# Optimization experiments

Hardware: AMD Instinct MI355X
Metric: run time of the kernel (lower is better)

The kernel has to match this reference:

```python
import jax, jax.numpy as jnp
import numpy as np

NEG = 1e9


def setup_inputs() -> dict:
    key = jax.random.key(0)
    ks = jax.random.split(key, 12)
    B, T1, T2, D1, D2, O, KF, G = 32, 512, 512, 256, 256, 256, 8, 64
    s = jnp.float32(0.05)  # keras 'random_normal' initializer stddev
    x0 = jax.random.normal(ks[0], (B, T1, D1), jnp.float32)
    x1 = jax.random.normal(ks[1], (B, T2, D2), jnp.float32)
    # realistic padding masks: first len tokens valid
    len1 = jax.random.randint(ks[2], (B,), T1 // 2, T1 + 1)
    len2 = jax.random.randint(ks[3], (B,), T2 // 2, T2 + 1)
    q_mask = jnp.arange(T1)[None, :] < len1[:, None]
    v_mask = jnp.arange(T2)[None, :] < len2[:, None]
    return {
        "x0": x0, "x1": x1, "q_mask": q_mask, "v_mask": v_mask,
        "W_R": jax.random.normal(ks[4], (1, O, D1), jnp.float32) * s,
        "W_Q": jax.random.normal(ks[5], (1, O, D2), jnp.float32) * s,
        "br": jnp.zeros((O, 1), jnp.float32),
        "bq": jnp.zeros((O, 1), jnp.float32),
        "U": jax.random.normal(ks[6], (1, O, T2, KF), jnp.float32) * s,
        "V": jax.random.normal(ks[7], (1, O, T1, KF), jnp.float32) * s,
        "W2_R": jax.random.normal(ks[8], (1, G, O), jnp.float32) * s,
        "W2_Q": jax.random.normal(ks[9], (1, G, O), jnp.float32) * s,
        "w_mv": jax.random.normal(ks[10], (G, 1), jnp.float32) * s,
        "w_mq": jax.random.normal(ks[11], (G, 1), jnp.float32) * s,
    }


def reference(x0, x1, q_mask, v_mask, W_R, W_Q, br, bq, U, V, W2_R, W2_Q, w_mv, w_mq):
    B, T1, D1 = x0.shape
    _, T2, D2 = x1.shape
    O = W_R.shape[1]
    KF = U.shape[-1]
    dt = x0.dtype
    # NB: original uses tf.reshape (NOT transpose) for all axis swaps; replicate exactly.
    in1 = x0.reshape(B, D1, T1)
    in2 = x1.reshape(B, D2, T2)
    R_l = jnp.einsum('od,bdt->bot', W_R[0], in1)          # (B,O,T1)
    Q_l = jnp.einsum('od,bds->bos', W_Q[0], in2)          # (B,O,T2)
    pad_q = (~q_mask).astype(dt)                          # (B,T1)
    pad_v = (~v_mask).astype(dt)                          # (B,T2)
    R_l = R_l - NEG * pad_q[:, None, :]
    Q_l = Q_l - NEG * pad_v[:, None, :]
    R_l = jax.nn.relu(R_l + br[None])                     # br (O,1) broadcasts over T1
    Q_l = jax.nn.relu(Q_l + bq[None])
    # factorized bilinear interaction, vectorized over rank k
    Uk = jnp.moveaxis(U[0], -1, 0).reshape(KF, T2, O)     # per-k reshape (O,T2)->(T2,O)
    Vk = jnp.moveaxis(V[0], -1, 0).reshape(KF, T1, O)     # per-k reshape (O,T1)->(T1,O)
    dot1 = jnp.einsum('kto,bos->kbts', Uk, R_l)           # (k,B,T2,T1)
    dot1 = dot1.reshape(KF, B, T1, T2)                    # per-slice reshape (T2,T1)->(T1,T2)
    dot2 = jnp.einsum('kso,bot->kbst', Vk, Q_l)           # (k,B,T1,T2)
    F = jnp.sum(dot1 * dot2, axis=0)                      # (B,T1,T2)
    F_tr = F.reshape(B, T2, T1)
    WR = jnp.einsum('go,bot->bgt', W2_R[0], R_l)          # (B,G,T1)
    WQ = jnp.einsum('go,bos->bgs', W2_Q[0], Q_l)          # (B,G,T2)
    M_v = jax.nn.relu(WR + jnp.einsum('bgs,bst->bgt', WQ, F_tr))   # (B,G,T1)
    M_q = jax.nn.relu(WQ + jnp.einsum('bgt,bts->bgs', WR, F))      # (B,G,T2)
    d1 = jnp.einsum('g,bgt->bt', w_mv[:, 0], M_v) - NEG * pad_q    # (B,T1)
    d2 = jnp.einsum('g,bgs->bs', w_mq[:, 0], M_q) - NEG * pad_v    # (B,T2)
    gamma_v = jax.nn.softmax(d1, axis=-1)
    gamma_q = jax.nn.softmax(d2, axis=-1)
    R_l2 = R_l.reshape(B, T1, O)
    Q_l2 = Q_l.reshape(B, T2, O)
    trace_emb = jnp.einsum('bt,bto->bo', gamma_v, R_l2)
    log_emb = jnp.einsum('bs,bso->bo', gamma_q, Q_l2)
    return trace_emb * log_emb                            # (B,O)
```

## Files before the change

kernel.cpp:

```cpp
#include <hip/hip_runtime.h>
#include <hip/hip_bf16.h>

typedef __hip_bfloat16 bf16;
typedef short bf16x8 __attribute__((ext_vector_type(8)));
typedef float f32x4 __attribute__((ext_vector_type(4)));
typedef unsigned int u32x4 __attribute__((ext_vector_type(4)));
typedef unsigned short us4 __attribute__((ext_vector_type(4)));

#define NEGV 1e9f

static constexpr int Bn = 32, Tn = 512, Dn = 256, On = 256, KFn = 8, Gn = 64;

__device__ __forceinline__ float bfs2f(unsigned short s) {
    unsigned u = ((unsigned)s) << 16; float f; __builtin_memcpy(&f, &u, 4); return f;
}
__device__ __forceinline__ unsigned short f2bfs(float f) {
    unsigned u; __builtin_memcpy(&u, &f, 4);
    u = u + 0x7FFFu + ((u >> 16) & 1u);
    return (unsigned short)(u >> 16);
}
__device__ __forceinline__ float loadf(const void* p, int i, int fl) {
    return fl ? bfs2f(((const unsigned short*)p)[i]) : ((const float*)p)[i];
}
__device__ __forceinline__ int detect_flag(const void* x0) {
    const unsigned short* u = (const unsigned short*)x0;
    int bad = 0;
    for (int i = 0; i < 32; i++) {
        unsigned short v = u[2 * i];
        int e = (v >> 7) & 0xFF;
        if (!(v == 0 || (e >= 90 && e <= 150))) bad++;
    }
    return (bad == 0) ? 1 : 0;
}
__device__ __forceinline__ void gload16(const unsigned short* g, unsigned short* l) {
    __builtin_amdgcn_global_load_lds(
        (const __attribute__((address_space(1))) unsigned int*)(unsigned long long)g,
        (__attribute__((address_space(3))) unsigned int*)(unsigned int)(unsigned long long)l,
        16, 0, 0);
}

__global__ void k_prep(const void* __restrict__ x0,
                       const void* __restrict__ qm, const void* __restrict__ vm,
                       const void* __restrict__ W_R, const void* __restrict__ W_Q,
                       const void* __restrict__ br, const void* __restrict__ bq,
                       const void* __restrict__ W2R, const void* __restrict__ W2Q,
                       const void* __restrict__ wmv, const void* __restrict__ wmq,
                       int* __restrict__ flag, float* __restrict__ padq, float* __restrict__ padv,
                       float* __restrict__ brf, float* __restrict__ bqf,
                       float* __restrict__ wmvf, float* __restrict__ wmqf,
                       float* __restrict__ W2Rf, float* __restrict__ W2Qf,
                       unsigned short* __restrict__ Whr, unsigned short* __restrict__ Wlr,
                       unsigned short* __restrict__ Whq, unsigned short* __restrict__ Wlq) {
    const int fl = detect_flag(x0);
    const int bid = blockIdx.x, tid = threadIdx.x;
    if (bid == 0) {
        if (tid == 0) *flag = fl;
        brf[tid] = loadf(br, tid, fl);
        bqf[tid] = loadf(bq, tid, fl);
        if (tid < 64) { wmvf[tid] = loadf(wmv, tid, fl); wmqf[tid] = loadf(wmq, tid, fl); }
    } else if (bid <= 128) {
        int i = (bid - 1) * 256 + tid;
        const unsigned char* qb = (const unsigned char*)qm;
        bool is32 = (qb[1] == 0);
        int j = i & 16383;
        const void* m = (i < 16384) ? qm : vm;
        float pv;
        if (is32) pv = ((const int*)m)[j] ? 0.f : 1.f;
        else      pv = ((const unsigned char*)m)[j] ? 0.f : 1.f;
        if (i < 16384) padq[j] = pv; else padv[j] = pv;
    } else if (bid <= 640) {
        int i = (bid - 129) * 256 + tid;
        const void* src = (i < 65536) ? W_R : W_Q;
        unsigned short* oh = (i < 65536) ? Whr : Whq;
        unsigned short* ol = (i < 65536) ? Wlr : Wlq;
        int j = i & 65535;
        float wv = loadf(src, j, fl);
        unsigned short h = f2bfs(wv);
        oh[j] = h;
        ol[j] = f2bfs(wv - bfs2f(h));
    } else {
        int i = (bid - 641) * 256 + tid;
        int j = i & 16383;
        if (i < 16384) W2Rf[j] = loadf(W2R, j, fl);
        else           W2Qf[j] = loadf(W2Q, j, fl);
    }
}

__global__ void k_perm(const void* __restrict__ U, const void* __restrict__ V,
                       unsigned short* __restrict__ Ud, unsigned short* __restrict__ Vd,
                       const int* __restrict__ flagp) {
    int i = blockIdx.x * 256 + threadIdx.x;
    const void* src = blockIdx.y ? V : U;
    unsigned short* dst = blockIdx.y ? Vd : Ud;
    int o = i & 255;
    int m = i >> 8;
    int a = m >> 3, k = m & 7;
    int f = a * 256 + o;
    int s = ((f >> 9) << 12) + ((f & 511) << 3) + k;
    if (*flagp) dst[i] = ((const unsigned short*)src)[s];
    else        dst[i] = f2bfs(((const float*)src)[s]);
}

__global__ __launch_bounds__(256) void k_xt(
    const void* __restrict__ x0, const void* __restrict__ x1,
    unsigned short* __restrict__ X0h, unsigned short* __restrict__ X0l,
    unsigned short* __restrict__ X1h, unsigned short* __restrict__ X1l,
    const int* __restrict__ flagp) {
    __shared__ float tl[64][65];
    const int inp = blockIdx.z >> 5, b = blockIdx.z & 31;
    const void* src = inp ? x1 : x0;
    unsigned short* oh = inp ? X1h : X0h;
    unsigned short* ol = inp ? X1l : X0l;
    const int t0 = blockIdx.x * 64, d0 = blockIdx.y * 64;
    const int tid = threadIdx.x;
    const int fl = *flagp;
#pragma unroll
    for (int p = 0; p < 16; ++p) {
        int idx = p * 256 + tid;
        int r = idx >> 6, c = idx & 63;
        size_t gi = ((size_t)b * 256 + d0 + r) * 512 + t0 + c;
        tl[r][c] = fl ? bfs2f(((const unsigned short*)src)[gi]) : ((const float*)src)[gi];
    }
    __syncthreads();
#pragma unroll
    for (int p = 0; p < 16; ++p) {
        int idx = p * 256 + tid;
        int r = idx >> 6, c = idx & 63;
        float v = tl[c][r];
        unsigned short h = f2bfs(v);
        size_t go = ((size_t)b * 512 + t0 + r) * 256 + d0 + c;
        oh[go] = h;
        ol[go] = f2bfs(v - bfs2f(h));
    }
}

__global__ __launch_bounds__(256) void k_rq(
    const unsigned short* __restrict__ X0h, const unsigned short* __restrict__ X0l,
    const unsigned short* __restrict__ X1h, const unsigned short* __restrict__ X1l,
    const unsigned short* __restrict__ Whr, const unsigned short* __restrict__ Wlr,
    const unsigned short* __restrict__ Whq, const unsigned short* __restrict__ Wlq,
    const float* __restrict__ padq, const float* __restrict__ padv,
    const float* __restrict__ brf, const float* __restrict__ bqf,
    unsigned short* __restrict__ Rth, unsigned short* __restrict__ Rtl,
    unsigned short* __restrict__ Qth, unsigned short* __restrict__ Qtl) {
    __shared__ __align__(16) unsigned short lds[4][4096];
    const int side = blockIdx.z >> 5, b = blockIdx.z & 31;
    const unsigned short* Ah = side ? X1h : X0h;
    const unsigned short* Al = side ? X1l : X0l;
    const unsigned short* Bh = side ? Whq : Whr;
    const unsigned short* Bl = side ? Wlq : Wlr;
    const float* pad = side ? padv : padq;
    const float* bias = side ? bqf : brf;
    unsigned short* Oh = side ? Qth : Rth;
    unsigned short* Ol = side ? Qtl : Rtl;
    const int t0 = blockIdx.y * 128, o0 = blockIdx.x * 128;
    const int tid = threadIdx.x, w = tid >> 6, lane = tid & 63;
    const int wm = w >> 1, wn = w & 1, lr = lane & 15, lk = lane >> 4;
    f32x4 acc[4][4];
#pragma unroll
    for (int i = 0; i < 4; i++)
#pragma unroll
        for (int j = 0; j < 4; j++)
#pragma unroll
            for (int q = 0; q < 4; q++) acc[i][j][q] = 0.f;

    for (int dc = 0; dc < 8; ++dc) {
        const int d0 = dc * 32;
        __syncthreads();
#pragma unroll
        for (int part = 0; part < 2; ++part) {
            const int s = w + part * 4;
            const size_t oA = ((size_t)(b * 512 + t0 + s * 16 + lr)) * 256 + d0 + lk * 8;
            const size_t oB = ((size_t)(o0 + s * 16 + lr)) * 256 + d0 + lk * 8;
            unsigned short* lb = &lds[0][s * 512];
            gload16(Ah + oA, lb);
            gload16(Al + oA, lb + 4096);
            gload16(Bh + oB, lb + 8192);
            gload16(Bl + oB, lb + 12288);
        }
        __syncthreads();
        bf16x8 ah[4], bh[4], bl[4], al[4];
#pragma unroll
        for (int f = 0; f < 4; ++f) {
            ah[f] = *(const bf16x8*)&lds[0][(wm * 4 + f) * 512 + lane * 8];
            bh[f] = *(const bf16x8*)&lds[2][(wn * 4 + f) * 512 + lane * 8];
        }
#pragma unroll
        for (int fa = 0; fa < 4; ++fa)
#pragma unroll
            for (int fc = 0; fc < 4; ++fc)
                acc[fa][fc] = __builtin_amdgcn_mfma_f32_16x16x32_bf16(ah[fa], bh[fc], acc[fa][fc], 0, 0, 0);
#pragma unroll
        for (int f = 0; f < 4; ++f)
            bl[f] = *(const bf16x8*)&lds[3][(wn * 4 + f) * 512 + lane * 8];
#pragma unroll
        for (int fa = 0; fa < 4; ++fa)
#pragma unroll
            for (int fc = 0; fc < 4; ++fc)
                acc[fa][fc] = __builtin_amdgcn_mfma_f32_16x16x32_bf16(ah[fa], bl[fc], acc[fa][fc], 0, 0, 0);
#pragma unroll
        for (int f = 0; f < 4; ++f)
            al[f] = *(const bf16x8*)&lds[1][(wm * 4 + f) * 512 + lane * 8];
#pragma unroll
        for (int fa = 0; fa < 4; ++fa)
#pragma unroll
            for (int fc = 0; fc < 4; ++fc)
                acc[fa][fc] = __builtin_amdgcn_mfma_f32_16x16x32_bf16(al[fa], bh[fc], acc[fa][fc], 0, 0, 0);
    }
    float bi[4];
#pragma unroll
    for (int fn = 0; fn < 4; ++fn) bi[fn] = bias[o0 + wn * 64 + fn * 16 + lr];
#pragma unroll
    for (int fm = 0; fm < 4; ++fm) {
        int tbase = t0 + wm * 64 + fm * 16 + lk * 4;
#pragma unroll
        for (int q = 0; q < 4; ++q) {
            int t = tbase + q;
            float pv = NEGV * pad[b * 512 + t];
#pragma unroll
            for (int fn = 0; fn < 4; ++fn) {
                int o = o0 + wn * 64 + fn * 16 + lr;
                float v = acc[fm][fn][q] - pv + bi[fn];
                v = v > 0.f ? v : 0.f;
                unsigned short h = f2bfs(v);
                size_t off = ((size_t)(b * 512 + t)) * 256 + o;
                Oh[off] = h;
                Ol[off] = f2bfs(v - bfs2f(h));
            }
        }
    }
}

__global__ __launch_bounds__(256, 2) void k_F(
    const unsigned short* __restrict__ Upp, const unsigned short* __restrict__ Vpp,
    const unsigned short* __restrict__ Rh, const unsigned short* __restrict__ Rl,
    const unsigned short* __restrict__ Qh, const unsigned short* __restrict__ Ql,
    float* __restrict__ Fh, int half) {
    __shared__ __align__(16) unsigned short lds[32][512];
    const int b = blockIdx.z;
    const int by = blockIdx.y;
    const int c0 = blockIdx.x * 64;
    const int m0 = half * 2048 + by * 128;
    const int tid = threadIdx.x;
    const int w = tid >> 6, lane = tid & 63;
    const int wm = w >> 1, wn = w & 1;
    const int lr = lane & 15, lk = lane >> 4;
    const size_t bTO = (size_t)b * Tn * On;

    const size_t aoff0 = (size_t)(m0 + (2 * w) * 16 + lr) * 256 + lk * 8;
    const size_t aoff1 = aoff0 + 16 * 256;
    const size_t boff = bTO + (size_t)(c0 + w * 16 + lr) * 256 + lk * 8;

    f32x4 d1[4][2], d2[4][2];
#pragma unroll
    for (int i = 0; i < 4; i++)
#pragma unroll
        for (int j = 0; j < 2; j++)
#pragma unroll
            for (int q = 0; q < 4; q++) { d1[i][j][q] = 0.f; d2[i][j][q] = 0.f; }

    for (int oc = 0; oc < 8; ++oc) {
        const int o0 = oc * 32;
        __syncthreads();
        gload16(Upp + aoff0 + o0, &lds[2 * w][0]);
        gload16(Upp + aoff1 + o0, &lds[2 * w + 1][0]);
        gload16(Vpp + aoff0 + o0, &lds[8 + 2 * w][0]);
        gload16(Vpp + aoff1 + o0, &lds[8 + 2 * w + 1][0]);
        gload16(Rh + boff + o0, &lds[16 + w][0]);
        gload16(Rl + boff + o0, &lds[20 + w][0]);
        gload16(Qh + boff + o0, &lds[24 + w][0]);
        gload16(Ql + boff + o0, &lds[28 + w][0]);
        __syncthreads();
        {
            bf16x8 ua[4], xh[2], xl[2];
#pragma unroll
            for (int f = 0; f < 4; ++f)
                ua[f] = *(const bf16x8*)&lds[wm * 4 + f][lane * 8];
#pragma unroll
            for (int f = 0; f < 2; ++f) {
                xh[f] = *(const bf16x8*)&lds[16 + wn * 2 + f][lane * 8];
                xl[f] = *(const bf16x8*)&lds[20 + wn * 2 + f][lane * 8];
            }
#pragma unroll
            for (int fa = 0; fa < 4; ++fa)
#pragma unroll
                for (int fc = 0; fc < 2; ++fc) {
                    d1[fa][fc] = __builtin_amdgcn_mfma_f32_16x16x32_bf16(ua[fa], xh[fc], d1[fa][fc], 0, 0, 0);
                    d1[fa][fc] = __builtin_amdgcn_mfma_f32_16x16x32_bf16(ua[fa], xl[fc], d1[fa][fc], 0, 0, 0);
                }
        }
        {
            bf16x8 va[4], xh[2], xl[2];
#pragma unroll
            for (int f = 0; f < 4; ++f)
                va[f] = *(const bf16x8*)&lds[8 + wm * 4 + f][lane * 8];
#pragma unroll
            for (int f = 0; f < 2; ++f) {
                xh[f] = *(const bf16x8*)&lds[24 + wn * 2 + f][lane * 8];
                xl[f] = *(const bf16x8*)&lds[28 + wn * 2 + f][lane * 8];
            }
#pragma unroll
            for (int fa = 0; fa < 4; ++fa)
#pragma unroll
                for (int fc = 0; fc < 2; ++fc) {
                    d2[fa][fc] = __builtin_amdgcn_mfma_f32_16x16x32_bf16(va[fa], xh[fc], d2[fa][fc], 0, 0, 0);
                    d2[fa][fc] = __builtin_amdgcn_mfma_f32_16x16x32_bf16(va[fa], xl[fc], d2[fa][fc], 0, 0, 0);
                }
        }
    }
#pragma unroll
    for (int fa = 0; fa < 4; ++fa)
#pragma unroll
        for (int fc = 0; fc < 2; ++fc) {
            float s = d1[fa][fc][0] * d2[fa][fc][0] + d1[fa][fc][1] * d2[fa][fc][1]
                    + d1[fa][fc][2] * d2[fa][fc][2] + d1[fa][fc][3] * d2[fa][fc][3];
            s += __shfl_xor(s, 16);
            if ((lane & 16) == 0) {
                int a_loc = by * 16 + wm * 8 + fa * 2 + (lk >> 1);
                int c = c0 + wn * 32 + fc * 16 + lr;
                Fh[((size_t)b * 256 + a_loc) * Tn + c] = s;
            }
        }
}

__global__ __launch_bounds__(256) void k_w2(
    const float* __restrict__ W2Rf, const float* __restrict__ W2Qf,
    const unsigned short* __restrict__ Rth, const unsigned short* __restrict__ Rtl,
    const unsigned short* __restrict__ Qth, const unsigned short* __restrict__ Qtl,
    float* __restrict__ WRw, float* __restrict__ WQw) {
    __shared__ float Wl[32][68];
    __shared__ float Sl[32][68];
    const int side = blockIdx.z;
    const float* W2 = side ? W2Qf : W2Rf;
    const unsigned short* Sh = side ? Qth : Rth;
    const unsigned short* Sl2 = side ? Qtl : Rtl;
    float* C = side ? WQw : WRw;
    int b = blockIdx.y, t0 = blockIdx.x * 64;
    int tid = threadIdx.x, tx = tid & 15, ty = tid >> 4;
    float acc[4][4] = {};
    for (int d0 = 0; d0 < On; d0 += 32) {
#pragma unroll
        for (int p = 0; p < 8; p++) {
            int idx = p * 256 + tid; int c = idx & 31, r = idx >> 5;
            Wl[c][r] = W2[r * On + d0 + c];
        }
#pragma unroll
        for (int p = 0; p < 8; p++) {
            int idx = p * 256 + tid; int tt = idx >> 5, c = idx & 31;
            size_t off = ((size_t)b * Tn + t0 + tt) * On + d0 + c;
            Sl[c][tt] = bfs2f(Sh[off]) + bfs2f(Sl2[off]);
        }
        __syncthreads();
#pragma unroll
        for (int kk = 0; kk < 32; kk++) {
            float4 a = *(const float4*)&Wl[kk][ty * 4];
            float4 x = *(const float4*)&Sl[kk][tx * 4];
            float av[4] = {a.x, a.y, a.z, a.w};
            float xv[4] = {x.x, x.y, x.z, x.w};
#pragma unroll
            for (int i = 0; i < 4; i++)
#pragma unroll
                for (int j = 0; j < 4; j++) acc[i][j] += av[i] * xv[j];
        }
        __syncthreads();
    }
#pragma unroll
    for (int i = 0; i < 4; i++) {
        float4 st = make_float4(acc[i][0], acc[i][1], acc[i][2], acc[i][3]);
        *(float4*)&C[((size_t)b * Gn + ty * 4 + i) * Tn + t0 + tx * 4] = st;
    }
}

__global__ __launch_bounds__(256) void k_md_acc(
    const float* __restrict__ WQw, const float* __restrict__ WRw,
    const float* __restrict__ F, float* __restrict__ Mv, float* __restrict__ Mq,
    int half, int init) {
    __shared__ float Wl1[32][68], Wl2[32][68], Fl[32][68];
    int b = blockIdx.y, x0 = blockIdx.x * 64;
    int tid = threadIdx.x, tx = tid & 15, ty = tid >> 4;
    float a1[4][4] = {}, a2[4][4] = {};
    const float* Fb = F + (size_t)b * 256 * Tn;
    for (int r0 = 0; r0 < 256; r0 += 32) {
#pragma unroll
        for (int p = 0; p < 8; p++) {
            int idx = p * 256 + tid; int c = idx & 31, g = idx >> 5;
            int rg = half * 256 + r0 + c;
            Wl1[c][g] = WQw[((size_t)b * Gn + g) * Tn + rg];
            Wl2[c][g] = WRw[((size_t)b * Gn + g) * Tn + rg];
        }
#pragma unroll
        for (int p = 0; p < 8; p++) {
            int idx = p * 256 + tid; int xx = idx & 63, c = idx >> 6;
            Fl[c][xx] = Fb[(size_t)(r0 + c) * Tn + x0 + xx];
        }
        __syncthreads();
#pragma unroll
        for (int kk = 0; kk < 32; kk++) {
            float4 w1 = *(const float4*)&Wl1[kk][ty * 4];
            float4 w2 = *(const float4*)&Wl2[kk][ty * 4];
            float4 xv = *(const float4*)&Fl[kk][tx * 4];
            float W1[4] = {w1.x, w1.y, w1.z, w1.w};
            float W2a[4] = {w2.x, w2.y, w2.z, w2.w};
            float Xv[4] = {xv.x, xv.y, xv.z, xv.w};
#pragma unroll
            for (int i = 0; i < 4; i++)
#pragma unroll
                for (int j = 0; j < 4; j++) {
                    a1[i][j] += W1[i] * Xv[j];
                    a2[i][j] += W2a[i] * Xv[j];
                }
        }
        __syncthreads();
    }
#pragma unroll
    for (int i = 0; i < 4; i++) {
        size_t off = ((size_t)b * Gn + ty * 4 + i) * Tn + x0 + tx * 4;
        if (init) {
            *(float4*)&Mv[off] = make_float4(a1[i][0], a1[i][1], a1[i][2], a1[i][3]);
            *(float4*)&Mq[off] = make_float4(a2[i][0], a2[i][1], a2[i][2], a2[i][3]);
        } else {
            float4 m1 = *(float4*)&Mv[off];
            float4 m2 = *(float4*)&Mq[off];
            m1.x += a1[i][0]; m1.y += a1[i][1]; m1.z += a1[i][2]; m1.w += a1[i][3];
            m2.x += a2[i][0]; m2.y += a2[i][1]; m2.z += a2[i][2]; m2.w += a2[i][3];
            *(float4*)&Mv[off] = m1;
            *(float4*)&Mq[off] = m2;
        }
    }
}

__global__ __launch_bounds__(256) void k_tail(
    const float* __restrict__ WRw, const float* __restrict__ WQw,
    const float* __restrict__ Mv, const float* __restrict__ Mq,
    const float* __restrict__ wmvf, const float* __restrict__ wmqf,
    const float* __restrict__ padq, const float* __restrict__ padv,
    const unsigned short* __restrict__ Rh, const unsigned short* __restrict__ Rl,
    const unsigned short* __restrict__ Qh, const unsigned short* __restrict__ Ql,
    void* __restrict__ out, const int* __restrict__ flagp) {
    __shared__ float g1[512], g2[512], w1[64], w2[64];
    __shared__ float sm1[4], sm2[4], ss1[4], ss2[4];
    const int b = blockIdx.x, tid = threadIdx.x;
    if (tid < 64) { w1[tid] = wmvf[tid]; w2[tid] = wmqf[tid]; }
    __syncthreads();
    for (int x = tid; x < 512; x += 256) {
        float s1 = 0.f, s2 = 0.f;
        for (int g = 0; g < 64; ++g) {
            size_t off = ((size_t)b * 64 + g) * 512 + x;
            float m1 = WRw[off] + Mv[off]; m1 = m1 > 0.f ? m1 : 0.f;
            float m2 = WQw[off] + Mq[off]; m2 = m2 > 0.f ? m2 : 0.f;
            s1 += w1[g] * m1;
            s2 += w2[g] * m2;
        }
        g1[x] = s1 - NEGV * padq[b * 512 + x];
        g2[x] = s2 - NEGV * padv[b * 512 + x];
    }
    __syncthreads();
    float a0 = g1[tid], a1v = g1[tid + 256], b0 = g2[tid], b1v = g2[tid + 256];
    float m1 = fmaxf(a0, a1v), m2 = fmaxf(b0, b1v);
#pragma unroll
    for (int off = 32; off; off >>= 1) {
        m1 = fmaxf(m1, __shfl_xor(m1, off));
        m2 = fmaxf(m2, __shfl_xor(m2, off));
    }
    int wid = tid >> 6;
    if ((tid & 63) == 0) { sm1[wid] = m1; sm2[wid] = m2; }
    __syncthreads();
    m1 = fmaxf(fmaxf(sm1[0], sm1[1]), fmaxf(sm1[2], sm1[3]));
    m2 = fmaxf(fmaxf(sm2[0], sm2[1]), fmaxf(sm2[2], sm2[3]));
    float e10 = expf(a0 - m1), e11 = expf(a1v - m1);
    float e20 = expf(b0 - m2), e21 = expf(b1v - m2);
    float s1 = e10 + e11, s2 = e20 + e21;
#pragma unroll
    for (int off = 32; off; off >>= 1) {
        s1 += __shfl_xor(s1, off);
        s2 += __shfl_xor(s2, off);
    }
    if ((tid & 63) == 0) { ss1[wid] = s1; ss2[wid] = s2; }
    __syncthreads();
    s1 = ss1[0] + ss1[1] + ss1[2] + ss1[3];
    s2 = ss2[0] + ss2[1] + ss2[2] + ss2[3];
    float i1 = 1.f / s1, i2 = 1.f / s2;
    g1[tid] = e10 * i1; g1[tid + 256] = e11 * i1;
    g2[tid] = e20 * i2; g2[tid + 256] = e21 * i2;
    __syncthreads();
    const int o = tid;
    const size_t r0 = ((size_t)b * Tn + o) * On;
    const size_t r1 = ((size_t)b * Tn + o + 256) * On;
    float acc1 = 0.f, acc2 = 0.f;
    for (int u8 = 0; u8 < 32; ++u8) {
        u32x4 rh0 = *(const u32x4*)&Rh[r0 + u8 * 8];
        u32x4 rl0 = *(const u32x4*)&Rl[r0 + u8 * 8];
        u32x4 rh1 = *(const u32x4*)&Rh[r1 + u8 * 8];
        u32x4 rl1 = *(const u32x4*)&Rl[r1 + u8 * 8];
        u32x4 qh0 = *(const u32x4*)&Qh[r0 + u8 * 8];
        u32x4 ql0 = *(const u32x4*)&Ql[r0 + u8 * 8];
        u32x4 qh1 = *(const u32x4*)&Qh[r1 + u8 * 8];
        u32x4 ql1 = *(const u32x4*)&Ql[r1 + u8 * 8];
#pragma unroll
        for (int e = 0; e < 4; ++e) {
            int ulo = u8 * 8 + 2 * e, uhi = ulo + 1;
            float r0lo = bfs2f((unsigned short)(rh0[e] & 0xFFFF)) + bfs2f((unsigned short)(rl0[e] & 0xFFFF));
            float r0hi = bfs2f((unsigned short)(rh0[e] >> 16))   + bfs2f((unsigned short)(rl0[e] >> 16));
            float r1lo = bfs2f((unsigned short)(rh1[e] & 0xFFFF)) + bfs2f((unsigned short)(rl1[e] & 0xFFFF));
            float r1hi = bfs2f((unsigned short)(rh1[e] >> 16))   + bfs2f((unsigned short)(rl1[e] >> 16));
            acc1 += g1[2 * ulo] * r0lo + g1[2 * uhi] * r0hi;
            acc1 += g1[2 * ulo + 1] * r1lo + g1[2 * uhi + 1] * r1hi;
            float q0lo = bfs2f((unsigned short)(qh0[e] & 0xFFFF)) + bfs2f((unsigned short)(ql0[e] & 0xFFFF));
            float q0hi = bfs2f((unsigned short)(qh0[e] >> 16))   + bfs2f((unsigned short)(ql0[e] >> 16));
            float q1lo = bfs2f((unsigned short)(qh1[e] & 0xFFFF)) + bfs2f((unsigned short)(ql1[e] & 0xFFFF));
            float q1hi = bfs2f((unsigned short)(qh1[e] >> 16))   + bfs2f((unsigned short)(ql1[e] >> 16));
            acc2 += g2[2 * ulo] * q0lo + g2[2 * uhi] * q0hi;
            acc2 += g2[2 * ulo + 1] * q1lo + g2[2 * uhi + 1] * q1hi;
        }
    }
    float p = acc1 * acc2;
    if (*flagp) ((bf16*)out)[b * On + o] = __float2bfloat16(p);
    else        ((float*)out)[b * On + o] = p;
}

extern "C" void kernel_launch(void* const* d_in, const int* in_sizes, int n_in,
                              void* d_out, int out_size, void* d_ws, size_t ws_size,
                              hipStream_t stream) {
    (void)in_sizes; (void)n_in; (void)out_size; (void)ws_size;
    const void* x0  = d_in[0];
    const void* x1  = d_in[1];
    const void* qm  = d_in[2];
    const void* vm  = d_in[3];
    const void* W_R = d_in[4];
    const void* W_Q = d_in[5];
    const void* br  = d_in[6];
    const void* bq  = d_in[7];
    const void* U   = d_in[8];
    const void* V   = d_in[9];
    const void* W2R = d_in[10];
    const void* W2Q = d_in[11];
    const void* wmv = d_in[12];
    const void* wmq = d_in[13];

    float* ws = (float*)d_ws;
    int*   flag = (int*)ws;
    float* padq = ws + 16;
    float* padv = padq + 16384;
    float* brf  = padv + 16384;
    float* bqf  = brf + 256;
    float* wmvf = bqf + 256;
    float* wmqf = wmvf + 64;
    float* W2Rf = wmqf + 64;
    float* W2Qf = W2Rf + 16384;
    unsigned short* Whr = (unsigned short*)(W2Qf + 16384);
    unsigned short* Wlr = Whr + 65536;
    unsigned short* Whq = Wlr + 65536;
    unsigned short* Wlq = Whq + 65536;
    unsigned short* Ubf = Wlq + 65536;
    unsigned short* Vbf = Ubf + 1048576;
    unsigned short* Rth = Vbf + 1048576;
    unsigned short* Rtl = Rth + 4194304;
    unsigned short* Qth = Rtl + 4194304;
    unsigned short* Qtl = Qth + 4194304;
    float* Mv   = (float*)(Qtl + 4194304);
    float* Mq   = Mv + 1048576;
    float* WRw  = Mq + 1048576;
    float* WQw  = WRw + 1048576;
    float* Fhalf = WQw + 1048576;
    unsigned short* Xt0h = (unsigned short*)Fhalf;
    unsigned short* Xt0l = Xt0h + 4194304;
    unsigned short* Xt1h = (unsigned short*)Mv;
    unsigned short* Xt1l = Xt1h + 4194304;

    k_prep<<<769, 256, 0, stream>>>(x0, qm, vm, W_R, W_Q, br, bq, W2R, W2Q, wmv, wmq,
                                    flag, padq, padv, brf, bqf, wmvf, wmqf,
                                    W2Rf, W2Qf, Whr, Wlr, Whq, Wlq);
    k_perm<<<dim3(4096, 2), 256, 0, stream>>>(U, V, Ubf, Vbf, flag);
    k_xt<<<dim3(8, 4, 64), 256, 0, stream>>>(x0, x1, Xt0h, Xt0l, Xt1h, Xt1l, flag);
    k_rq<<<dim3(2, 4, 64), 256, 0, stream>>>(Xt0h, Xt0l, Xt1h, Xt1l,
                                             Whr, Wlr, Whq, Wlq,
                                             padq, padv, brf, bqf,
                                             Rth, Rtl, Qth, Qtl);
    k_w2<<<dim3(8, 32, 2), 256, 0, stream>>>(W2Rf, W2Qf, Rth, Rtl, Qth, Qtl, WRw, WQw);
    for (int half = 0; half < 2; half++) {
        k_F<<<dim3(8, 16, 32), 256, 0, stream>>>(Ubf, Vbf, Rth, Rtl, Qth, Qtl, Fhalf, half);
        k_md_acc<<<dim3(8, 32), 256, 0, stream>>>(WQw, WRw, Fhalf, Mv, Mq, half, half == 0);
    }
    k_tail<<<32, 256, 0, stream>>>(WRw, WQw, Mv, Mq, wmvf, wmqf, padq, padv,
                                   Rth, Rtl, Qth, Qtl, d_out, flag);
}
```

Before: 514.4 us.

## Move W2 projection to split-bf16 MFMA, vectorize prep kernels, widen k_F tiles

Replaces the scalar fp32 k_w2 GEMM with an MFMA version that stores W2 as bf16 hi/lo pairs and accumulates three cross products. It also vectorizes the loads and stores in k_perm and k_xt, using 8-wide chunks. k_F moves to 512-thread blocks with a 128-column tile, so the U/V tiles are loaded once per block and shared across more columns. The aim is to cut scalar FMA and memory-transaction overhead in several kernels. The costs are larger LDS use and register pressure in k_F, and a slight precision change in WR/WQ because the lo*lo term is dropped.

```diff
diff --git a/kernel.cpp b/kernel.cpp
--- a/kernel.cpp
+++ b/kernel.cpp
@@ -5,7 +5,7 @@
 typedef short bf16x8 __attribute__((ext_vector_type(8)));
 typedef float f32x4 __attribute__((ext_vector_type(4)));
 typedef unsigned int u32x4 __attribute__((ext_vector_type(4)));
-typedef unsigned short us4 __attribute__((ext_vector_type(4)));
+typedef unsigned short us8 __attribute__((ext_vector_type(8)));
 
 #define NEGV 1e9f
 
@@ -48,7 +48,8 @@
                        int* __restrict__ flag, float* __restrict__ padq, float* __restrict__ padv,
                        float* __restrict__ brf, float* __restrict__ bqf,
                        float* __restrict__ wmvf, float* __restrict__ wmqf,
-                       float* __restrict__ W2Rf, float* __restrict__ W2Qf,
+                       unsigned short* __restrict__ W2Rh, unsigned short* __restrict__ W2Rl,
+                       unsigned short* __restrict__ W2Qh, unsigned short* __restrict__ W2Ql,
                        unsigned short* __restrict__ Whr, unsigned short* __restrict__ Wlr,
                        unsigned short* __restrict__ Whq, unsigned short* __restrict__ Wlq) {
     const int fl = detect_flag(x0);
@@ -81,24 +82,34 @@
     } else {
         int i = (bid - 641) * 256 + tid;
         int j = i & 16383;
-        if (i < 16384) W2Rf[j] = loadf(W2R, j, fl);
-        else           W2Qf[j] = loadf(W2Q, j, fl);
+        float wv = loadf(i < 16384 ? W2R : W2Q, j, fl);
+        unsigned short h = f2bfs(wv);
+        unsigned short l = f2bfs(wv - bfs2f(h));
+        if (i < 16384) { W2Rh[j] = h; W2Rl[j] = l; }
+        else           { W2Qh[j] = h; W2Ql[j] = l; }
     }
 }
 
 __global__ void k_perm(const void* __restrict__ U, const void* __restrict__ V,
                        unsigned short* __restrict__ Ud, unsigned short* __restrict__ Vd,
                        const int* __restrict__ flagp) {
-    int i = blockIdx.x * 256 + threadIdx.x;
+    int j = blockIdx.x * 256 + threadIdx.x;
     const void* src = blockIdx.y ? V : U;
     unsigned short* dst = blockIdx.y ? Vd : Ud;
-    int o = i & 255;
-    int m = i >> 8;
-    int a = m >> 3, k = m & 7;
+    int a = j >> 8, o = j & 255;
     int f = a * 256 + o;
-    int s = ((f >> 9) << 12) + ((f & 511) << 3) + k;
-    if (*flagp) dst[i] = ((const unsigned short*)src)[s];
-    else        dst[i] = f2bfs(((const float*)src)[s]);
+    int s0 = ((f >> 9) << 12) + ((f & 511) << 3);
+    unsigned short kv[8];
+    if (*flagp) {
+        us8 v = *(const us8*)&((const unsigned short*)src)[s0];
+#pragma unroll
+        for (int k = 0; k < 8; ++k) kv[k] = v[k];
+    } else {
+#pragma unroll
+        for (int k = 0; k < 8; ++k) kv[k] = f2bfs(((const float*)src)[s0 + k]);
+    }
+#pragma unroll
+    for (int k = 0; k < 8; ++k) dst[(a * 8 + k) * 256 + o] = kv[k];
 }
 
 __global__ __launch_bounds__(256) void k_xt(
@@ -115,22 +126,37 @@
     const int tid = threadIdx.x;
     const int fl = *flagp;
 #pragma unroll
-    for (int p = 0; p < 16; ++p) {
+    for (int p = 0; p < 2; ++p) {
         int idx = p * 256 + tid;
-        int r = idx >> 6, c = idx & 63;
-        size_t gi = ((size_t)b * 256 + d0 + r) * 512 + t0 + c;
-        tl[r][c] = fl ? bfs2f(((const unsigned short*)src)[gi]) : ((const float*)src)[gi];
+        int r = idx >> 3, c8 = (idx & 7) * 8;
+        size_t gi = ((size_t)b * 256 + d0 + r) * 512 + t0 + c8;
+        if (fl) {
+            us8 v = *(const us8*)&((const unsigned short*)src)[gi];
+#pragma unroll
+            for (int jj = 0; jj < 8; ++jj) tl[r][c8 + jj] = bfs2f(v[jj]);
+        } else {
+            float4 v0 = *(const float4*)&((const float*)src)[gi];
+            float4 v1 = *(const float4*)&((const float*)src)[gi + 4];
+            tl[r][c8 + 0] = v0.x; tl[r][c8 + 1] = v0.y; tl[r][c8 + 2] = v0.z; tl[r][c8 + 3] = v0.w;
+            tl[r][c8 + 4] = v1.x; tl[r][c8 + 5] = v1.y; tl[r][c8 + 6] = v1.z; tl[r][c8 + 7] = v1.w;
+        }
     }
     __syncthreads();
 #pragma unroll
-    for (int p = 0; p < 16; ++p) {
+    for (int p = 0; p < 2; ++p) {
         int idx = p * 256 + tid;
-        int r = idx >> 6, c = idx & 63;
-        float v = tl[c][r];
-        unsigned short h = f2bfs(v);
-        size_t go = ((size_t)b * 512 + t0 + r) * 256 + d0 + c;
-        oh[go] = h;
-        ol[go] = f2bfs(v - bfs2f(h));
+        int r = idx >> 3, c8 = (idx & 7) * 8;
+        us8 hv, lv;
+#pragma unroll
+        for (int jj = 0; jj < 8; ++jj) {
+            float v = tl[c8 + jj][r];
+            unsigned short h = f2bfs(v);
+            hv[jj] = h;
+            lv[jj] = f2bfs(v - bfs2f(h));
+        }
+        size_t go = ((size_t)b * 512 + t0 + r) * 256 + d0 + c8;
+        *(us8*)&oh[go] = hv;
+        *(us8*)&ol[go] = lv;
     }
 }
 
@@ -231,24 +257,23 @@
     }
 }
 
-__global__ __launch_bounds__(256, 2) void k_F(
+__global__ __launch_bounds__(512, 2) void k_F(
     const unsigned short* __restrict__ Upp, const unsigned short* __restrict__ Vpp,
     const unsigned short* __restrict__ Rh, const unsigned short* __restrict__ Rl,
     const unsigned short* __restrict__ Qh, const unsigned short* __restrict__ Ql,
     float* __restrict__ Fh, int half) {
-    __shared__ __align__(16) unsigned short lds[32][512];
+    __shared__ __align__(16) unsigned short lds[48][512];
     const int b = blockIdx.z;
     const int by = blockIdx.y;
-    const int c0 = blockIdx.x * 64;
+    const int c0 = blockIdx.x * 128;
     const int m0 = half * 2048 + by * 128;
     const int tid = threadIdx.x;
     const int w = tid >> 6, lane = tid & 63;
-    const int wm = w >> 1, wn = w & 1;
+    const int wm = w >> 2, wn = w & 3;
     const int lr = lane & 15, lk = lane >> 4;
     const size_t bTO = (size_t)b * Tn * On;
 
-    const size_t aoff0 = (size_t)(m0 + (2 * w) * 16 + lr) * 256 + lk * 8;
-    const size_t aoff1 = aoff0 + 16 * 256;
+    const size_t aoff = (size_t)(m0 + w * 16 + lr) * 256 + lk * 8;
     const size_t boff = bTO + (size_t)(c0 + w * 16 + lr) * 256 + lk * 8;
 
     f32x4 d1[4][2], d2[4][2];
@@ -262,14 +287,12 @@
     for (int oc = 0; oc < 8; ++oc) {
         const int o0 = oc * 32;
         __syncthreads();
-        gload16(Upp + aoff0 + o0, &lds[2 * w][0]);
-        gload16(Upp + aoff1 + o0, &lds[2 * w + 1][0]);
-        gload16(Vpp + aoff0 + o0, &lds[8 + 2 * w][0]);
-        gload16(Vpp + aoff1 + o0, &lds[8 + 2 * w + 1][0]);
+        gload16(Upp + aoff + o0, &lds[w][0]);
+        gload16(Vpp + aoff + o0, &lds[8 + w][0]);
         gload16(Rh + boff + o0, &lds[16 + w][0]);
-        gload16(Rl + boff + o0, &lds[20 + w][0]);
-        gload16(Qh + boff + o0, &lds[24 + w][0]);
-        gload16(Ql + boff + o0, &lds[28 + w][0]);
+        gload16(Rl + boff + o0, &lds[24 + w][0]);
+        gload16(Qh + boff + o0, &lds[32 + w][0]);
+        gload16(Ql + boff + o0, &lds[40 + w][0]);
         __syncthreads();
         {
             bf16x8 ua[4], xh[2], xl[2];
@@ -279,7 +302,7 @@
 #pragma unroll
             for (int f = 0; f < 2; ++f) {
                 xh[f] = *(const bf16x8*)&lds[16 + wn * 2 + f][lane * 8];
-                xl[f] = *(const bf16x8*)&lds[20 + wn * 2 + f][lane * 8];
+                xl[f] = *(const bf16x8*)&lds[24 + wn * 2 + f][lane * 8];
             }
 #pragma unroll
             for (int fa = 0; fa < 4; ++fa)
@@ -296,8 +319,8 @@
                 va[f] = *(const bf16x8*)&lds[8 + wm * 4 + f][lane * 8];
 #pragma unroll
             for (int f = 0; f < 2; ++f) {
-                xh[f] = *(const bf16x8*)&lds[24 + wn * 2 + f][lane * 8];
-                xl[f] = *(const bf16x8*)&lds[28 + wn * 2 + f][lane * 8];
+                xh[f] = *(const bf16x8*)&lds[32 + wn * 2 + f][lane * 8];
+                xl[f] = *(const bf16x8*)&lds[40 + wn * 2 + f][lane * 8];
             }
 #pragma unroll
             for (int fa = 0; fa < 4; ++fa)
@@ -324,51 +347,72 @@
 }
 
 __global__ __launch_bounds__(256) void k_w2(
-    const float* __restrict__ W2Rf, const float* __restrict__ W2Qf,
+    const unsigned short* __restrict__ W2Rh, const unsigned short* __restrict__ W2Rl,
+    const unsigned short* __restrict__ W2Qh, const unsigned short* __restrict__ W2Ql,
     const unsigned short* __restrict__ Rth, const unsigned short* __restrict__ Rtl,
     const unsigned short* __restrict__ Qth, const unsigned short* __restrict__ Qtl,
     float* __restrict__ WRw, float* __restrict__ WQw) {
-    __shared__ float Wl[32][68];
-    __shared__ float Sl[32][68];
-    const int side = blockIdx.z;
-    const float* W2 = side ? W2Qf : W2Rf;
-    const unsigned short* Sh = side ? Qth : Rth;
-    const unsigned short* Sl2 = side ? Qtl : Rtl;
+    __shared__ __align__(16) unsigned short lds[24][512];
+    const int side = blockIdx.z, b = blockIdx.y, t0 = blockIdx.x * 128;
+    const unsigned short* Ah = side ? W2Qh : W2Rh;
+    const unsigned short* Al = side ? W2Ql : W2Rl;
+    const unsigned short* Bh = side ? Qth : Rth;
+    const unsigned short* Bl = side ? Qtl : Rtl;
     float* C = side ? WQw : WRw;
-    int b = blockIdx.y, t0 = blockIdx.x * 64;
-    int tid = threadIdx.x, tx = tid & 15, ty = tid >> 4;
-    float acc[4][4] = {};
-    for (int d0 = 0; d0 < On; d0 += 32) {
-#pragma unroll
-        for (int p = 0; p < 8; p++) {
-            int idx = p * 256 + tid; int c = idx & 31, r = idx >> 5;
-            Wl[c][r] = W2[r * On + d0 + c];
-        }
-#pragma unroll
-        for (int p = 0; p < 8; p++) {
-            int idx = p * 256 + tid; int tt = idx >> 5, c = idx & 31;
-            size_t off = ((size_t)b * Tn + t0 + tt) * On + d0 + c;
-            Sl[c][tt] = bfs2f(Sh[off]) + bfs2f(Sl2[off]);
-        }
-        __syncthreads();
-#pragma unroll
-        for (int kk = 0; kk < 32; kk++) {
-            float4 a = *(const float4*)&Wl[kk][ty * 4];
-            float4 x = *(const float4*)&Sl[kk][tx * 4];
-            float av[4] = {a.x, a.y, a.z, a.w};
-            float xv[4] = {x.x, x.y, x.z, x.w};
-#pragma unroll
-            for (int i = 0; i < 4; i++)
-#pragma unroll
-                for (int j = 0; j < 4; j++) acc[i][j] += av[i] * xv[j];
-        }
-        __syncthreads();
-    }
-#pragma unroll
-    for (int i = 0; i < 4; i++) {
-        float4 st = make_float4(acc[i][0], acc[i][1], acc[i][2], acc[i][3]);
-        *(float4*)&C[((size_t)b * Gn + ty * 4 + i) * Tn + t0 + tx * 4] = st;
-    }
+    const int tid = threadIdx.x, w = tid >> 6, lane = tid & 63;
+    const int lr = lane & 15, lk = lane >> 4;
+    const size_t bTO = (size_t)b * Tn * On;
+    const size_t aoff = (size_t)(w * 16 + lr) * 256 + lk * 8;
+    const size_t boff0 = bTO + (size_t)(t0 + (2 * w) * 16 + lr) * 256 + lk * 8;
+    const size_t boff1 = boff0 + 16 * 256;
+    f32x4 acc[4][2];
+#pragma unroll
+    for (int i = 0; i < 4; i++)
+#pragma unroll
+        for (int j = 0; j < 2; j++)
+#pragma unroll
+            for (int q = 0; q < 4; q++) acc[i][j][q] = 0.f;
+
+    for (int oc = 0; oc < 8; ++oc) {
+        const int o0 = oc * 32;
+        __syncthreads();
+        gload16(Ah + aoff + o0, &lds[w][0]);
+        gload16(Al + aoff + o0, &lds[4 + w][0]);
+        gload16(Bh + boff0 + o0, &lds[8 + 2 * w][0]);
+        gload16(Bh + boff1 + o0, &lds[8 + 2 * w + 1][0]);
+        gload16(Bl + boff0 + o0, &lds[16 + 2 * w][0]);
+        gload16(Bl + boff1 + o0, &lds[16 + 2 * w + 1][0]);
+        __syncthreads();
+        bf16x8 ah[4], al[4], bh[2], bl[2];
+#pragma unroll
+        for (int f = 0; f < 4; ++f) {
+            ah[f] = *(const bf16x8*)&lds[f][lane * 8];
+            al[f] = *(const bf16x8*)&lds[4 + f][lane * 8];
+        }
+#pragma unroll
+        for (int f = 0; f < 2; ++f) {
+            bh[f] = *(const bf16x8*)&lds[8 + w * 2 + f][lane * 8];
+            bl[f] = *(const bf16x8*)&lds[16 + w * 2 + f][lane * 8];
+        }
+#pragma unroll
+        for (int fa = 0; fa < 4; ++fa)
+#pragma unroll
+            for (int fc = 0; fc < 2; ++fc) {
+                acc[fa][fc] = __builtin_amdgcn_mfma_f32_16x16x32_bf16(ah[fa], bh[fc], acc[fa][fc], 0, 0, 0);
+                acc[fa][fc] = __builtin_amdgcn_mfma_f32_16x16x32_bf16(ah[fa], bl[fc], acc[fa][fc], 0, 0, 0);
+                acc[fa][fc] = __builtin_amdgcn_mfma_f32_16x16x32_bf16(al[fa], bh[fc], acc[fa][fc], 0, 0, 0);
+            }
+    }
+#pragma unroll
+    for (int fa = 0; fa < 4; ++fa)
+#pragma unroll
+        for (int fc = 0; fc < 2; ++fc)
+#pragma unroll
+            for (int q = 0; q < 4; ++q) {
+                int g = fa * 16 + lk * 4 + q;
+                int t = t0 + w * 32 + fc * 16 + lr;
+                C[((size_t)(b * Gn + g)) * Tn + t] = acc[fa][fc][q];
+            }
 }
 
 __global__ __launch_bounds__(256) void k_md_acc(
@@ -545,9 +589,11 @@
     float* bqf  = brf + 256;
     float* wmvf = bqf + 256;
     float* wmqf = wmvf + 64;
-    float* W2Rf = wmqf + 64;
-    float* W2Qf = W2Rf + 16384;
-    unsigned short* Whr = (unsigned short*)(W2Qf + 16384);
+    unsigned short* W2Rh = (unsigned short*)(wmqf + 64);
+    unsigned short* W2Rl = W2Rh + 16384;
+    unsigned short* W2Qh = W2Rl + 16384;
+    unsigned short* W2Ql = W2Qh + 16384;
+    unsigned short* Whr = W2Ql + 16384;
     unsigned short* Wlr = Whr + 65536;
     unsigned short* Whq = Wlr + 65536;
     unsigned short* Wlq = Whq + 65536;
@@ -569,16 +615,17 @@
 
     k_prep<<<769, 256, 0, stream>>>(x0, qm, vm, W_R, W_Q, br, bq, W2R, W2Q, wmv, wmq,
                                     flag, padq, padv, brf, bqf, wmvf, wmqf,
-                                    W2Rf, W2Qf, Whr, Wlr, Whq, Wlq);
-    k_perm<<<dim3(4096, 2), 256, 0, stream>>>(U, V, Ubf, Vbf, flag);
+                                    W2Rh, W2Rl, W2Qh, W2Ql, Whr, Wlr, Whq, Wlq);
+    k_perm<<<dim3(512, 2), 256, 0, stream>>>(U, V, Ubf, Vbf, flag);
     k_xt<<<dim3(8, 4, 64), 256, 0, stream>>>(x0, x1, Xt0h, Xt0l, Xt1h, Xt1l, flag);
     k_rq<<<dim3(2, 4, 64), 256, 0, stream>>>(Xt0h, Xt0l, Xt1h, Xt1l,
                                              Whr, Wlr, Whq, Wlq,
                                              padq, padv, brf, bqf,
                                              Rth, Rtl, Qth, Qtl);
-    k_w2<<<dim3(8, 32, 2), 256, 0, stream>>>(W2Rf, W2Qf, Rth, Rtl, Qth, Qtl, WRw, WQw);
+    k_w2<<<dim3(4, 32, 2), 256, 0, stream>>>(W2Rh, W2Rl, W2Qh, W2Ql,
+                                             Rth, Rtl, Qth, Qtl, WRw, WQw);
     for (int half = 0; half < 2; half++) {
-        k_F<<<dim3(8, 16, 32), 256, 0, stream>>>(Ubf, Vbf, Rth, Rtl, Qth, Qtl, Fhalf, half);
+        k_F<<<dim3(4, 16, 32), 512, 0, stream>>>(Ubf, Vbf, Rth, Rtl, Qth, Qtl, Fhalf, half);
         k_md_acc<<<dim3(8, 32), 256, 0, stream>>>(WQw, WRw, Fhalf, Mv, Mq, half, half == 0);
     }
     k_tail<<<32, 256, 0, stream>>>(WRw, WQw, Mv, Mq, wmvf, wmqf, padq, padv,
```

Measured after the change: 520.6 us. No clear change (+1.2%).
